# Kernel tuning notes

Hardware: AMD Instinct MI355X
Metric: run time of the kernel (lower is better)

## Reference

```python
import jax, jax.numpy as jnp
import numpy as np

B, S, E = 4096, 200, 128
ATT_H, MLP_H = 128, 256


def _glorot(key, shape):
    fan_in, fan_out = shape[0], shape[1]
    lim = np.sqrt(6.0 / (fan_in + fan_out)).astype(np.float32)
    return jax.random.uniform(key, shape, jnp.float32, -lim, lim)


def setup_inputs() -> dict:
    key = jax.random.key(0)
    ks = jax.random.split(key, 10)
    return {
        "behavior_emb": jax.random.normal(ks[0], (B, S, E), jnp.float32),
        "candidate_emb": jax.random.normal(ks[1], (B, E), jnp.float32),
        "fc1_w": _glorot(ks[2], (2 * E, ATT_H)),
        "fc1_b": jnp.zeros((ATT_H,), jnp.float32),
        "fc2_w": _glorot(ks[3], (ATT_H, 1)),
        "fc2_b": jnp.zeros((1,), jnp.float32),
        "mlp1_w": _glorot(ks[4], (2 * E, MLP_H)),
        "mlp1_b": jnp.zeros((MLP_H,), jnp.float32),
        "mlp2_w": _glorot(ks[5], (MLP_H, 1)),
        "mlp2_b": jnp.zeros((1,), jnp.float32),
    }


def reference(behavior_emb, candidate_emb, fc1_w, fc1_b, fc2_w, fc2_b,
              mlp1_w, mlp1_b, mlp2_w, mlp2_b):
    # Attention unit: split fc1 weight so we avoid materializing the concat.
    # concat([beh, cand]) @ fc1_w == beh @ W_b + cand @ W_c
    W_b, W_c = fc1_w[:E], fc1_w[E:]
    h = jax.nn.relu(jnp.einsum('bse,eh->bsh', behavior_emb, W_b)
                    + (candidate_emb @ W_c)[:, None, :] + fc1_b)  # [B,S,H]
    scores = jnp.einsum('bsh,h->bs', h, fc2_w[:, 0]) + fc2_b[0]   # [B,S]
    attn = jax.nn.softmax(scores, axis=-1)                         # [B,S]
    user_interest = jnp.einsum('bse,bs->be', behavior_emb, attn)   # [B,E]
    # MLP head
    x = jnp.concatenate([user_interest, candidate_emb], axis=1)    # [B,2E]
    z = jax.nn.relu(x @ mlp1_w + mlp1_b)
    logit = (z @ mlp2_w + mlp2_b)[:, 0]                            # [B]
    return logit
```

## Files before the change

kernel.cpp:

```cpp
#include <hip/hip_runtime.h>
#include <hip/hip_bf16.h>
#include <stdint.h>

#define BN   4096
#define SN   200
#define EN   128
#define HN   128
#define RPB  8
#define NBLK (BN / RPB)

typedef __attribute__((ext_vector_type(8)))  short  short8;
typedef __attribute__((ext_vector_type(16))) float  floatx16;

#define SYNC_LGK() do {                                            \
    asm volatile("s_waitcnt lgkmcnt(0)\n\ts_barrier" ::: "memory");\
    __builtin_amdgcn_sched_barrier(0);                             \
  } while (0)
#define ASM_VMCNT0() do {                                          \
    asm volatile("s_waitcnt vmcnt(0)" ::: "memory");               \
    __builtin_amdgcn_sched_barrier(0);                             \
  } while (0)

__device__ __forceinline__ unsigned short f2bf(float f) {
  union { float f; uint32_t u; } c; c.f = f;
  uint32_t r = c.u + 0x7fffu + ((c.u >> 16) & 1u);
  return (unsigned short)(r >> 16);
}
__device__ __forceinline__ float bf2f(unsigned short h) {
  union { uint32_t u; float f; } c; c.u = ((uint32_t)h) << 16;
  return c.f;
}
__device__ __forceinline__ uint32_t pk2(float x, float y) {
#if defined(__has_builtin) && __has_builtin(__builtin_amdgcn_cvt_pk_bf16_f32)
  typedef __bf16 bf16x2 __attribute__((ext_vector_type(2)));
  return __builtin_bit_cast(uint32_t, __builtin_amdgcn_cvt_pk_bf16_f32(x, y));
#else
  return (uint32_t)f2bf(x) | ((uint32_t)f2bf(y) << 16);
#endif
}
__device__ __forceinline__ float bcast_lane(float v, int l) {
  return __builtin_bit_cast(float, __builtin_amdgcn_readlane(__builtin_bit_cast(int, v), l));
}

__device__ __forceinline__ int aoff(int s, int g) {
  return s * 256 + (((g ^ (s & 15)) << 4));
}

__device__ __forceinline__ void issue_row(const float* __restrict__ src, int tid,
                                          float4 (&va)[13]) {
  #pragma unroll
  for (int u = 0; u < 12; ++u) {
    int q = u * 512 + tid;
    va[u] = *(const float4*)(src + (q >> 5) * EN + ((q & 31) << 2));
  }
  if (tid < 256) {
    int q = 6144 + tid;
    va[12] = *(const float4*)(src + (q >> 5) * EN + ((q & 31) << 2));
  }
}

__device__ __forceinline__ void convert_row(unsigned short* dst, int tid,
                                            const float4 (&va)[13]) {
  #pragma unroll
  for (int u = 0; u < 12; ++u) {
    int q = u * 512 + tid, s = q >> 5, e4 = (q & 31) << 2;
    uint2 pk = make_uint2(pk2(va[u].x, va[u].y), pk2(va[u].z, va[u].w));
    *(uint2*)((char*)dst + s * 256 + ((((e4 >> 3) ^ (s & 15))) << 4) + ((e4 & 7) << 1)) = pk;
  }
  if (tid < 256) {
    int q = 6144 + tid, s = q >> 5, e4 = (q & 31) << 2;
    uint2 pk = make_uint2(pk2(va[12].x, va[12].y), pk2(va[12].z, va[12].w));
    *(uint2*)((char*)dst + s * 256 + ((((e4 >> 3) ^ (s & 15))) << 4) + ((e4 & 7) << 1)) = pk;
  }
}

__global__ void din_prep(const float* __restrict__ fc1w, short8* __restrict__ ws_afr) {
  const int t    = blockIdx.x & 7;
  const int wv   = blockIdx.x >> 3;
  const int lane = threadIdx.x;
  const int half = lane >> 5;
  const int hcol = wv * 32 + (lane & 31);
  short8 fr;
  #pragma unroll
  for (int j = 0; j < 8; ++j) {
    int e = t * 16 + half * 8 + j;
    fr[j] = (short)f2bf(fc1w[e * HN + hcol]);
  }
  ws_afr[((wv * 8 + t) << 6) + lane] = fr;
}

__global__ __launch_bounds__(512, 2)
void din_attn(const float* __restrict__ behavior, const float* __restrict__ cand,
              const float* __restrict__ fc1w, const float* __restrict__ fc1b,
              const float* __restrict__ fc2w, const short8* __restrict__ ws_afr,
              float* __restrict__ ws_ui) {
  __shared__ unsigned short Abuf[2][SN * EN];
  __shared__ float scores_s[SN];
  __shared__ float cvec_all[RPB][HN];
  __shared__ float cand_all[RPB][EN];
  __shared__ float ui_s[EN];

  const int tid  = threadIdx.x;
  const int wv   = tid >> 6;
  const int lane = tid & 63;
  const int half = lane >> 5;
  const int l31  = lane & 31;
  const int ht   = wv & 3;
  const int stb  = (wv >> 2) ? 4 : 0;
  const int ste  = (wv >> 2) ? 7 : 4;

  const int base = blockIdx.x * RPB;

  if (tid < SN) scores_s[tid] = 0.f;
  if (tid < EN) ui_s[tid] = 0.f;
  if (tid < RPB * EN / 4)
    ((float4*)cand_all)[tid] = ((const float4*)(cand + (size_t)base * EN))[tid];

  short8 afr[8];
  #pragma unroll
  for (int t = 0; t < 8; ++t) afr[t] = ws_afr[((ht * 8 + t) << 6) + lane];
  float wmul[16];
  #pragma unroll
  for (int i = 0; i < 16; ++i) {
    int hr = ht * 32 + (i & 3) + ((i >> 2) << 3) + (half << 2);
    wmul[i] = fc2w[hr];
  }
  __syncthreads();

  float4 va[13];
  issue_row(behavior + (size_t)base * SN * EN, tid, va);

  {
    const int h  = tid & 127;
    const int r0 = tid >> 7;
    float a0 = fc1b[h], a1 = a0;
    const float* wc = fc1w + (size_t)EN * HN + h;
    #pragma unroll 8
    for (int e = 0; e < EN; ++e) {
      float w = wc[(size_t)e * HN];
      a0 = fmaf(cand_all[r0][e],     w, a0);
      a1 = fmaf(cand_all[r0 + 4][e], w, a1);
    }
    cvec_all[r0][h]     = a0;
    cvec_all[r0 + 4][h] = a1;
  }

  convert_row(Abuf[0], tid, va);
  __syncthreads();

  for (int it = 0; it < RPB; ++it) {
    const int cur = it & 1;

    if (it + 1 < RPB) {
      issue_row(behavior + (size_t)(base + it + 1) * SN * EN, tid, va);
      __builtin_amdgcn_sched_barrier(0);
    }

    float cadd[16];
    #pragma unroll
    for (int i = 0; i < 16; ++i) {
      int hr = ht * 32 + (i & 3) + ((i >> 2) << 3) + (half << 2);
      cadd[i] = cvec_all[it][hr];
    }
    for (int st = stb; st < ste; ++st) {
      floatx16 acc;
      #pragma unroll
      for (int i = 0; i < 16; ++i) acc[i] = cadd[i];
      const int srow = st * 32 + l31;
      const int sr   = (srow < SN) ? srow : (SN - 1);
      #pragma unroll
      for (int t = 0; t < 8; ++t) {
        const short8 bfr = *(const short8*)((const char*)Abuf[cur] + aoff(sr, 2 * t + half));
        acc = __builtin_amdgcn_mfma_f32_32x32x16_bf16(afr[t], bfr, acc, 0, 0, 0);
      }
      float part = 0.f;
      #pragma unroll
      for (int i = 0; i < 16; ++i)
        part = fmaf(fmaxf(acc[i], 0.f), wmul[i], part);
      part += __shfl_xor(part, 32, 64);
      if (lane < 32 && srow < SN) atomicAdd(&scores_s[srow], part);
    }
    SYNC_LGK();

    if (wv == 0) {
      float v0[4];
      #pragma unroll
      for (int k = 0; k < 4; ++k) {
        int s = k * 64 + lane;
        v0[k] = (s < SN) ? scores_s[s] : -3.0e38f;
      }
      float m = fmaxf(fmaxf(v0[0], v0[1]), fmaxf(v0[2], v0[3]));
      #pragma unroll
      for (int off = 32; off >= 1; off >>= 1) m = fmaxf(m, __shfl_xor(m, off, 64));
      float e0[4], sum = 0.f;
      #pragma unroll
      for (int k = 0; k < 4; ++k) { e0[k] = __expf(v0[k] - m); sum += e0[k]; }
      #pragma unroll
      for (int off = 32; off >= 1; off >>= 1) sum += __shfl_xor(sum, off, 64);
      float inv = 1.0f / sum;
      #pragma unroll
      for (int k = 0; k < 4; ++k) {
        int s = k * 64 + lane;
        if (s < SN) scores_s[s] = e0[k] * inv;
      }
    }
    SYNC_LGK();

    {
      const int g  = tid & 15;
      const int sg = tid >> 4;
      float ua[8] = {0.f,0.f,0.f,0.f,0.f,0.f,0.f,0.f};
      for (int s = sg; s < SN; s += 32) {
        float a = scores_s[s];
        const short8 bv = *(const short8*)((const char*)Abuf[cur] + aoff(s, g));
        #pragma unroll
        for (int j = 0; j < 8; ++j) ua[j] = fmaf(a, bf2f((unsigned short)bv[j]), ua[j]);
      }
      #pragma unroll
      for (int j = 0; j < 8; ++j) {
        ua[j] += __shfl_xor(ua[j], 16, 64);
        ua[j] += __shfl_xor(ua[j], 32, 64);
      }
      if (lane < 16) {
        #pragma unroll
        for (int j = 0; j < 8; ++j) atomicAdd(&ui_s[(g << 3) + j], ua[j]);
      }
    }
    SYNC_LGK();

    if (tid < EN) {
      ws_ui[(size_t)(base + it) * EN + tid] = ui_s[tid];
      ui_s[tid] = 0.f;
    } else if (tid >= 256 && tid < 256 + SN) {
      scores_s[tid - 256] = 0.f;
    }

    if (it + 1 < RPB) {
      ASM_VMCNT0();
      convert_row(Abuf[cur ^ 1], tid, va);
    }
    SYNC_LGK();
  }
}

__global__ __launch_bounds__(256, 4)
void din_mlp(const float* __restrict__ ws_ui, const float* __restrict__ cand,
             const float* __restrict__ w1, const float* __restrict__ b1,
             const float* __restrict__ w2, const float* __restrict__ b2,
             float* __restrict__ out) {
  const int tid  = threadIdx.x;
  const int lane = tid & 63;
  const int wv   = tid >> 6;
  const int r0   = blockIdx.x * 4;

  float xr[4][4];
  #pragma unroll
  for (int r = 0; r < 4; ++r) {
    #pragma unroll
    for (int c = 0; c < 4; ++c) {
      int i = c * 64 + lane;
      int row = r0 + r;
      xr[r][c] = (i < 128) ? ws_ui[row * 128 + i] : cand[row * 128 + (i - 128)];
    }
  }

  const int j = tid;
  const float bj = b1[j];
  float acc[4] = {bj, bj, bj, bj};

  #pragma unroll
  for (int c = 0; c < 4; ++c) {
    #pragma unroll 8
    for (int il = 0; il < 64; ++il) {
      float w = w1[(c * 64 + il) * 256 + j];
      #pragma unroll
      for (int r = 0; r < 4; ++r)
        acc[r] = fmaf(bcast_lane(xr[r][c], il), w, acc[r]);
    }
  }

  const float w2j = w2[j];
  float part[4];
  #pragma unroll
  for (int r = 0; r < 4; ++r) part[r] = fmaxf(acc[r], 0.f) * w2j;
  #pragma unroll
  for (int off = 32; off >= 1; off >>= 1) {
    #pragma unroll
    for (int r = 0; r < 4; ++r) part[r] += __shfl_xor(part[r], off, 64);
  }

  __shared__ float red[4][4];
  if (lane == 0) {
    #pragma unroll
    for (int r = 0; r < 4; ++r) red[wv][r] = part[r];
  }
  __syncthreads();
  if (tid < 4)
    out[r0 + tid] = red[0][tid] + red[1][tid] + red[2][tid] + red[3][tid] + b2[0];
}

extern "C" void kernel_launch(void* const* d_in, const int* in_sizes, int n_in,
                              void* d_out, int out_size, void* d_ws, size_t ws_size,
                              hipStream_t stream) {
  const float* behavior = (const float*)d_in[0];
  const float* cand     = (const float*)d_in[1];
  const float* fc1w     = (const float*)d_in[2];
  const float* fc1b     = (const float*)d_in[3];
  const float* fc2w     = (const float*)d_in[4];
  const float* m1w      = (const float*)d_in[6];
  const float* m1b      = (const float*)d_in[7];
  const float* m2w      = (const float*)d_in[8];
  const float* m2b      = (const float*)d_in[9];
  float* outp    = (float*)d_out;
  float* ws_ui   = (float*)d_ws;
  short8* ws_afr = (short8*)((char*)d_ws + (size_t)BN * EN * 4);

  din_prep<<<32, 64, 0, stream>>>(fc1w, ws_afr);
  din_attn<<<NBLK, 512, 0, stream>>>(behavior, cand, fc1w, fc1b, fc2w, ws_afr, ws_ui);
  din_mlp<<<BN / 4, 256, 0, stream>>>(ws_ui, cand, m1w, m1b, m2w, m2b, outp);
}
```

Before: 634.0 us.

## Fuse prep, attention and MLP head into one kernel with 16 rows per block

Merges the three launches into a single kernel. The fc1 weight fragments are now converted to bf16 inside each block, and the MLP head is computed at the end of each block from user-interest vectors held in shared memory. Rows per block go from 8 to 16, which halves the grid to 256 blocks and spreads the MLP and the weight conversion over more rows. This removes two launches and the global round trip for the user-interest vectors. The cost is less parallelism per block, since 256 blocks may not fill all CUs at 2 blocks per CU, plus redundant per-block weight conversion and a longer serial tail.

```diff
diff --git a/kernel.cpp b/kernel.cpp
--- a/kernel.cpp
+++ b/kernel.cpp
@@ -6,7 +6,8 @@
 #define SN   200
 #define EN   128
 #define HN   128
-#define RPB  8
+#define MHN  256
+#define RPB  16
 #define NBLK (BN / RPB)
 
 typedef __attribute__((ext_vector_type(8)))  short  short8;
@@ -38,9 +39,6 @@
   return (uint32_t)f2bf(x) | ((uint32_t)f2bf(y) << 16);
 #endif
 }
-__device__ __forceinline__ float bcast_lane(float v, int l) {
-  return __builtin_bit_cast(float, __builtin_amdgcn_readlane(__builtin_bit_cast(int, v), l));
-}
 
 __device__ __forceinline__ int aoff(int s, int g) {
   return s * 256 + (((g ^ (s & 15)) << 4));
@@ -74,31 +72,19 @@
   }
 }
 
-__global__ void din_prep(const float* __restrict__ fc1w, short8* __restrict__ ws_afr) {
-  const int t    = blockIdx.x & 7;
-  const int wv   = blockIdx.x >> 3;
-  const int lane = threadIdx.x;
-  const int half = lane >> 5;
-  const int hcol = wv * 32 + (lane & 31);
-  short8 fr;
-  #pragma unroll
-  for (int j = 0; j < 8; ++j) {
-    int e = t * 16 + half * 8 + j;
-    fr[j] = (short)f2bf(fc1w[e * HN + hcol]);
-  }
-  ws_afr[((wv * 8 + t) << 6) + lane] = fr;
-}
-
 __global__ __launch_bounds__(512, 2)
-void din_attn(const float* __restrict__ behavior, const float* __restrict__ cand,
-              const float* __restrict__ fc1w, const float* __restrict__ fc1b,
-              const float* __restrict__ fc2w, const short8* __restrict__ ws_afr,
-              float* __restrict__ ws_ui) {
+void din_fused(const float* __restrict__ behavior, const float* __restrict__ cand,
+               const float* __restrict__ fc1w, const float* __restrict__ fc1b,
+               const float* __restrict__ fc2w,
+               const float* __restrict__ m1w, const float* __restrict__ m1b,
+               const float* __restrict__ m2w, const float* __restrict__ m2b,
+               float* __restrict__ out) {
   __shared__ unsigned short Abuf[2][SN * EN];
   __shared__ float scores_s[SN];
   __shared__ float cvec_all[RPB][HN];
   __shared__ float cand_all[RPB][EN];
-  __shared__ float ui_s[EN];
+  __shared__ float ui_all[RPB][EN];
+  __shared__ float red8[8][8];
 
   const int tid  = threadIdx.x;
   const int wv   = tid >> 6;
@@ -112,37 +98,47 @@
   const int base = blockIdx.x * RPB;
 
   if (tid < SN) scores_s[tid] = 0.f;
-  if (tid < EN) ui_s[tid] = 0.f;
-  if (tid < RPB * EN / 4)
-    ((float4*)cand_all)[tid] = ((const float4*)(cand + (size_t)base * EN))[tid];
+  #pragma unroll
+  for (int i = tid; i < RPB * EN; i += 512) ((float*)ui_all)[i] = 0.f;
+  ((float4*)cand_all)[tid] = ((const float4*)(cand + (size_t)base * EN))[tid];
+  __syncthreads();
+
+  float4 va[13];
+  issue_row(behavior + (size_t)base * SN * EN, tid, va);
 
   short8 afr[8];
   #pragma unroll
-  for (int t = 0; t < 8; ++t) afr[t] = ws_afr[((ht * 8 + t) << 6) + lane];
+  for (int t = 0; t < 8; ++t) {
+    #pragma unroll
+    for (int j = 0; j < 8; ++j) {
+      int e = t * 16 + half * 8 + j;
+      afr[t][j] = (short)f2bf(fc1w[e * HN + ht * 32 + l31]);
+    }
+  }
   float wmul[16];
   #pragma unroll
   for (int i = 0; i < 16; ++i) {
     int hr = ht * 32 + (i & 3) + ((i >> 2) << 3) + (half << 2);
     wmul[i] = fc2w[hr];
   }
-  __syncthreads();
-
-  float4 va[13];
-  issue_row(behavior + (size_t)base * SN * EN, tid, va);
 
   {
     const int h  = tid & 127;
     const int r0 = tid >> 7;
-    float a0 = fc1b[h], a1 = a0;
+    float a0 = fc1b[h], a1 = a0, a2 = a0, a3 = a0;
     const float* wc = fc1w + (size_t)EN * HN + h;
     #pragma unroll 8
     for (int e = 0; e < EN; ++e) {
       float w = wc[(size_t)e * HN];
-      a0 = fmaf(cand_all[r0][e],     w, a0);
-      a1 = fmaf(cand_all[r0 + 4][e], w, a1);
-    }
-    cvec_all[r0][h]     = a0;
-    cvec_all[r0 + 4][h] = a1;
+      a0 = fmaf(cand_all[r0][e],      w, a0);
+      a1 = fmaf(cand_all[r0 + 4][e],  w, a1);
+      a2 = fmaf(cand_all[r0 + 8][e],  w, a2);
+      a3 = fmaf(cand_all[r0 + 12][e], w, a3);
+    }
+    cvec_all[r0][h]      = a0;
+    cvec_all[r0 + 4][h]  = a1;
+    cvec_all[r0 + 8][h]  = a2;
+    cvec_all[r0 + 12][h] = a3;
   }
 
   convert_row(Abuf[0], tid, va);
@@ -223,17 +219,12 @@
       }
       if (lane < 16) {
         #pragma unroll
-        for (int j = 0; j < 8; ++j) atomicAdd(&ui_s[(g << 3) + j], ua[j]);
-      }
-    }
-    SYNC_LGK();
-
-    if (tid < EN) {
-      ws_ui[(size_t)(base + it) * EN + tid] = ui_s[tid];
-      ui_s[tid] = 0.f;
-    } else if (tid >= 256 && tid < 256 + SN) {
-      scores_s[tid - 256] = 0.f;
-    }
+        for (int j = 0; j < 8; ++j) atomicAdd(&ui_all[it][(g << 3) + j], ua[j]);
+      }
+    }
+    SYNC_LGK();
+
+    if (tid < SN) scores_s[tid] = 0.f;
 
     if (it + 1 < RPB) {
       ASM_VMCNT0();
@@ -241,62 +232,49 @@
     }
     SYNC_LGK();
   }
-}
-
-__global__ __launch_bounds__(256, 4)
-void din_mlp(const float* __restrict__ ws_ui, const float* __restrict__ cand,
-             const float* __restrict__ w1, const float* __restrict__ b1,
-             const float* __restrict__ w2, const float* __restrict__ b2,
-             float* __restrict__ out) {
-  const int tid  = threadIdx.x;
-  const int lane = tid & 63;
-  const int wv   = tid >> 6;
-  const int r0   = blockIdx.x * 4;
-
-  float xr[4][4];
-  #pragma unroll
-  for (int r = 0; r < 4; ++r) {
-    #pragma unroll
-    for (int c = 0; c < 4; ++c) {
-      int i = c * 64 + lane;
-      int row = r0 + r;
-      xr[r][c] = (i < 128) ? ws_ui[row * 128 + i] : cand[row * 128 + (i - 128)];
-    }
-  }
-
-  const int j = tid;
-  const float bj = b1[j];
-  float acc[4] = {bj, bj, bj, bj};
-
-  #pragma unroll
-  for (int c = 0; c < 4; ++c) {
-    #pragma unroll 8
-    for (int il = 0; il < 64; ++il) {
-      float w = w1[(c * 64 + il) * 256 + j];
-      #pragma unroll
-      for (int r = 0; r < 4; ++r)
-        acc[r] = fmaf(bcast_lane(xr[r][c], il), w, acc[r]);
-    }
-  }
-
-  const float w2j = w2[j];
-  float part[4];
-  #pragma unroll
-  for (int r = 0; r < 4; ++r) part[r] = fmaxf(acc[r], 0.f) * w2j;
-  #pragma unroll
-  for (int off = 32; off >= 1; off >>= 1) {
-    #pragma unroll
-    for (int r = 0; r < 4; ++r) part[r] += __shfl_xor(part[r], off, 64);
-  }
-
-  __shared__ float red[4][4];
-  if (lane == 0) {
-    #pragma unroll
-    for (int r = 0; r < 4; ++r) red[wv][r] = part[r];
+
+  {
+    const int j  = tid & 255;
+    const int rh = tid >> 8;
+    const float bj = m1b[j];
+    float accm[8];
+    #pragma unroll
+    for (int r = 0; r < 8; ++r) accm[r] = bj;
+    #pragma unroll 4
+    for (int i = 0; i < 128; ++i) {
+      float w = m1w[i * MHN + j];
+      #pragma unroll
+      for (int r = 0; r < 8; ++r)
+        accm[r] = fmaf(ui_all[rh * 8 + r][i], w, accm[r]);
+    }
+    #pragma unroll 4
+    for (int i = 0; i < 128; ++i) {
+      float w = m1w[(128 + i) * MHN + j];
+      #pragma unroll
+      for (int r = 0; r < 8; ++r)
+        accm[r] = fmaf(cand_all[rh * 8 + r][i], w, accm[r]);
+    }
+    const float w2j = m2w[j];
+    float prt[8];
+    #pragma unroll
+    for (int r = 0; r < 8; ++r) prt[r] = fmaxf(accm[r], 0.f) * w2j;
+    #pragma unroll
+    for (int off = 32; off >= 1; off >>= 1) {
+      #pragma unroll
+      for (int r = 0; r < 8; ++r) prt[r] += __shfl_xor(prt[r], off, 64);
+    }
+    if (lane == 0) {
+      #pragma unroll
+      for (int r = 0; r < 8; ++r) red8[wv][r] = prt[r];
+    }
   }
   __syncthreads();
-  if (tid < 4)
-    out[r0 + tid] = red[0][tid] + red[1][tid] + red[2][tid] + red[3][tid] + b2[0];
+  if (tid < RPB) {
+    const int g = tid >> 3, rr = tid & 7;
+    float s = red8[g * 4 + 0][rr] + red8[g * 4 + 1][rr]
+            + red8[g * 4 + 2][rr] + red8[g * 4 + 3][rr];
+    out[base + tid] = s + m2b[0];
+  }
 }
 
 extern "C" void kernel_launch(void* const* d_in, const int* in_sizes, int n_in,
@@ -312,10 +290,7 @@
   const float* m2w      = (const float*)d_in[8];
   const float* m2b      = (const float*)d_in[9];
   float* outp    = (float*)d_out;
-  float* ws_ui   = (float*)d_ws;
-  short8* ws_afr = (short8*)((char*)d_ws + (size_t)BN * EN * 4);
-
-  din_prep<<<32, 64, 0, stream>>>(fc1w, ws_afr);
-  din_attn<<<NBLK, 512, 0, stream>>>(behavior, cand, fc1w, fc1b, fc2w, ws_afr, ws_ui);
-  din_mlp<<<BN / 4, 256, 0, stream>>>(ws_ui, cand, m1w, m1b, m2w, m2b, outp);
-}
+
+  din_fused<<<NBLK, 512, 0, stream>>>(behavior, cand, fc1w, fc1b, fc2w,
+                                      m1w, m1b, m2w, m2b, outp);
+}
```

After: 616.0 us. 2.8% less time.
